# Kernel tuning notes

Measured on AMD Instinct MI355X. Metric: run time of the kernel, lower is better.

Reference implementation:

```python
import jax, jax.numpy as jnp
import numpy as np

N, LH, PL = 512, 20, 10          # agents, history len, prediction len
H, E, NH, FF = 128, 64, 10, 2048  # rnn hidden, embedding, heads, ffn dim
D = H + 2                         # transformer d_model = 130
DH = D // NH                      # head dim = 13
DT = 0.1
NLAYERS = 3


def setup_inputs() -> dict:
    key = jax.random.key(0)
    ks = list(jax.random.split(key, 40))
    def rn(shape, s=0.02):
        return jax.random.normal(ks.pop(), shape, jnp.float32) * s
    Tracks = jax.random.normal(ks.pop(), (N, LH, 5), jnp.float32)
    Tracks = Tracks.at[:, :, 0].set(1.0)  # nonzero ids: all agents active every frame
    return dict(
        Tracks=Tracks,
        W_emb=rn((E, 4)), b_emb=jnp.zeros((E,), jnp.float32),
        W_ih=rn((4 * H, E)), W_hh=rn((4 * H, H)),
        b_ih=jnp.zeros((4 * H,), jnp.float32), b_hh=jnp.zeros((4 * H,), jnp.float32),
        enc_qkv_w=rn((NLAYERS, 3 * D, D)), enc_qkv_b=jnp.zeros((NLAYERS, 3 * D), jnp.float32),
        enc_out_w=rn((NLAYERS, D, D)), enc_out_b=jnp.zeros((NLAYERS, D), jnp.float32),
        enc_ff1_w=rn((NLAYERS, FF, D)), enc_ff1_b=jnp.zeros((NLAYERS, FF), jnp.float32),
        enc_ff2_w=rn((NLAYERS, D, FF)), enc_ff2_b=jnp.zeros((NLAYERS, D), jnp.float32),
        enc_ln1_s=jnp.ones((NLAYERS, D), jnp.float32), enc_ln1_b=jnp.zeros((NLAYERS, D), jnp.float32),
        enc_ln2_s=jnp.ones((NLAYERS, D), jnp.float32), enc_ln2_b=jnp.zeros((NLAYERS, D), jnp.float32),
        W_sp=rn((H, D)), b_sp=jnp.zeros((H,), jnp.float32),
        W_p1=rn((H, H)), b_p1=jnp.zeros((H,), jnp.float32),
        W_p2=rn((H, H)), b_p2=jnp.zeros((H,), jnp.float32),
        W_pl=rn((2, H)), b_pl=jnp.zeros((2,), jnp.float32),
    )


def _ln(x, s, b):
    m = jnp.mean(x, -1, keepdims=True)
    v = jnp.mean((x - m) ** 2, -1, keepdims=True)
    return (x - m) / jnp.sqrt(v + 1e-5) * s + b


def _mha(x, qkv_w, qkv_b, ow, ob):
    # x: [N, D] unbatched sequence of N agent tokens (torch unbatched semantics)
    qkv = x @ qkv_w.T + qkv_b
    q, k, v = jnp.split(qkv, 3, -1)
    def heads(t):
        return t.reshape(-1, NH, DH).transpose(1, 0, 2)  # [NH, N, DH]
    q, k, v = heads(q), heads(k), heads(v)
    scores = jnp.einsum('hnd,hmd->hnm', q, k) / jnp.sqrt(jnp.float32(DH))
    att = jax.nn.softmax(scores, -1)
    o = jnp.einsum('hnm,hmd->hnd', att, v).transpose(1, 0, 2).reshape(-1, D)
    return o @ ow.T + ob


def _forward(Tracks, W_emb, b_emb, W_ih, W_hh, b_ih, b_hh,
             enc_qkv_w, enc_qkv_b, enc_out_w, enc_out_b,
             enc_ff1_w, enc_ff1_b, enc_ff2_w, enc_ff2_b,
             enc_ln1_s, enc_ln1_b, enc_ln2_s, enc_ln2_b,
             W_sp, b_sp, W_p1, b_p1, W_p2, b_p2, W_pl, b_pl):
    def emb(x):
        return x @ W_emb.T + b_emb

    def lstm(x, h, c):  # torch LSTMCell, gate order i,f,g,o
        g = x @ W_ih.T + b_ih + h @ W_hh.T + b_hh
        i, f, gg, o = jnp.split(g, 4, -1)
        c2 = jax.nn.sigmoid(f) * c + jax.nn.sigmoid(i) * jnp.tanh(gg)
        return jax.nn.sigmoid(o) * jnp.tanh(c2), c2

    def sp(h, pos):  # sp_model: 3-layer post-norm transformer encoder + linear
        x = jnp.concatenate([h, pos], 1)  # [N, D]
        for j in range(NLAYERS):
            a = _mha(x, enc_qkv_w[j], enc_qkv_b[j], enc_out_w[j], enc_out_b[j])
            x = _ln(x + a, enc_ln1_s[j], enc_ln1_b[j])
            f = jax.nn.relu(x @ enc_ff1_w[j].T + enc_ff1_b[j]) @ enc_ff2_w[j].T + enc_ff2_b[j]
            x = _ln(x + f, enc_ln2_s[j], enc_ln2_b[j])
        return x @ W_sp.T + b_sp

    def rm_sp(inp, Sh, c):
        h2, c2 = lstm(emb(inp), Sh, c)
        return sp(h2, inp[:, :2]), c2

    n = Tracks.shape[0]
    inp0 = Tracks[:, 0, 1:]
    z = jnp.zeros((n, H), Tracks.dtype)
    h, c = lstm(emb(inp0), z, z)  # step-0 init (original processes step 0 twice)
    Sh = sp(h, inp0[:, :2])

    def step(carry, inp):
        Sh, c = carry
        Sh, c = rm_sp(inp, Sh, c)
        return (Sh, c), None

    (Sh, c), _ = jax.lax.scan(step, (Sh, c), jnp.moveaxis(Tracks[:, :, 1:], 1, 0))

    def pstep(carry, _):
        Sh, c, cf = carry
        x = jax.nn.relu(Sh @ W_p1.T + b_p1) + Sh
        x = jax.nn.relu(x @ W_p2.T + b_p2) + x
        a = x @ W_pl.T + b_pl                       # acceleration [N,2]
        v = a * DT + cf[:, 2:]                      # velocity update first (in-place order)
        pnew = a * (DT * DT / 2) + v * DT + cf[:, :2]
        out = jnp.concatenate([pnew, v], 1)
        Sh, c = rm_sp(out, Sh, c)
        return (Sh, c, out), out

    _, pre = jax.lax.scan(pstep, (Sh, c, Tracks[:, -1, 1:]), None, length=PL)
    return jnp.moveaxis(pre, 0, 1)  # [N, pre_len, 4]


def reference(Tracks, W_emb, b_emb, W_ih, W_hh, b_ih, b_hh,
              enc_qkv_w, enc_qkv_b, enc_out_w, enc_out_b,
              enc_ff1_w, enc_ff1_b, enc_ff2_w, enc_ff2_b,
              enc_ln1_s, enc_ln1_b, enc_ln2_s, enc_ln2_b,
              W_sp, b_sp, W_p1, b_p1, W_p2, b_p2, W_pl, b_pl):
    return _forward(Tracks, W_emb, b_emb, W_ih, W_hh, b_ih, b_hh,
                    enc_qkv_w, enc_qkv_b, enc_out_w, enc_out_b,
                    enc_ff1_w, enc_ff1_b, enc_ff2_w, enc_ff2_b,
                    enc_ln1_s, enc_ln1_b, enc_ln2_s, enc_ln2_b,
                    W_sp, b_sp, W_p1, b_p1, W_p2, b_p2, W_pl, b_pl)
```

## Files before the change

### kernel.cpp

```cpp
#include <hip/hip_runtime.h>


#define Nn 512
#define Dd 130
#define DP 132
#define Hh 128
#define Ee 64
#define FFf 2048
#define KG 192
#define TS 68

typedef float v4 __attribute__((ext_vector_type(4)));
typedef float v2 __attribute__((ext_vector_type(2)));

struct Args {
  const float *Tracks, *W_emb, *b_emb, *W_ih, *W_hh, *b_ih, *b_hh;
  const float *qkv_w, *qkv_b, *out_w, *out_b, *ff1_w, *ff1_b, *ff2_w, *ff2_b;
  const float *ln1_s, *ln1_b, *ln2_s, *ln2_b;
  const float *W_sp, *b_sp, *W_p1, *b_p1, *W_p2, *b_p2, *W_pl, *b_pl;
  float *X, *T, *Q, *Kb, *V, *O, *Sh, *C, *X1, *X2, *Y, *PART, *outp;
};

__device__ __forceinline__ float sigm(float x){ return 1.f/(1.f+__expf(-x)); }

#define LN_REDUCE(SCR) \
  { int row_=tid>>3, l8=tid&7; float s1=0.f, s2=0.f; \
    for (int k=0;k<17;k++){ int c=l8+8*k; if(c<Dd){ float v=(SCR)[row_*132+c]; s1+=v; s2+=v*v; } } \
    red1[row_*9+l8]=s1; red2_[row_*9+l8]=s2; } \
  __syncthreads(); \
  if (tid<64){ float s1=0.f,s2=0.f; \
    for (int k=0;k<8;k++){ s1+=red1[tid*9+k]; s2+=red2_[tid*9+k]; } \
    float m=s1/130.f; mu[tid]=m; inv[tid]=rsqrtf(s2/130.f-m*m+1e-5f); } \
  __syncthreads();

#define GEMM64(KK) \
  float acc[2][4] = {}; \
  { const float* xp = xs + 2*ig; \
    const float* wp = ws + 4*cg; \
    _Pragma("unroll 4") \
    for (int j=0;j<(KK);j++){ \
      v2 xv = *(const v2*)(xp + j*TS); \
      v4 wv = *(const v4*)(wp + j*TS); \
      _Pragma("unroll") \
      for (int aa=0;aa<2;aa++) \
        _Pragma("unroll") \
        for (int bb=0;bb<4;bb++) acc[aa][bb] += xv[aa]*wv[bb]; \
    } }

__global__ __launch_bounds__(512) void k_proj(Args a){
  int rg = blockIdx.x & 7, cs = blockIdx.x >> 3;
  int r0 = rg*64, c0 = cs*64;
  __shared__ alignas(16) float xs[Dd*TS];
  __shared__ alignas(16) float ws[Dd*TS];
  __shared__ float row[64*132];
  __shared__ float red1[64*9], red2_[64*9], mu[64], inv[64];
  int tid = threadIdx.x, cg = tid & 15, ig = tid >> 4;
  const float* f2b = a.ff2_b + 2*Dd;
  const float* lns = a.ln2_s + 2*Dd;
  const float* lnb = a.ln2_b + 2*Dd;
  for (int idx=tid; idx<64*Dd; idx+=512){ int c=idx/Dd, j=idx-c*Dd; ws[j*TS+c] = a.W_sp[(c0+c)*Dd+j]; }
  for (int idx=tid; idx<64*Dd; idx+=512){ int i=idx/Dd, j=idx-i*Dd;
    float sum = a.X[(r0+i)*DP+j] + f2b[j];
    for (int ksl=0;ksl<16;ksl++) sum += a.PART[(ksl*Nn + r0+i)*DP + j];
    row[i*132+j] = sum; }
  __syncthreads();
  LN_REDUCE(row)
  for (int idx=tid; idx<64*Dd; idx+=512){ int i=idx/Dd, j=idx-i*Dd;
    xs[j*TS+i] = (row[i*132+j]-mu[i])*inv[i]*lns[j] + lnb[j]; }
  __syncthreads();
  GEMM64(Dd)
  #pragma unroll
  for (int aa=0;aa<2;aa++){
    int r = r0 + 2*ig + aa, c = c0 + 4*cg;
    v4 o;
    #pragma unroll
    for (int bb=0;bb<4;bb++) o[bb] = acc[aa][bb] + a.b_sp[c+bb];
    *(v4*)&a.Sh[r*Hh+c] = o;
  }
}

__global__ __launch_bounds__(512) void k_tail(Args a, int p){
  int r0 = blockIdx.x*64;
  __shared__ alignas(16) float xs[Dd*TS];
  __shared__ alignas(16) float ws[Dd*TS];
  __shared__ float A[64*132];
  __shared__ float B[64*132];
  __shared__ float red1[64*9], red2_[64*9], mu[64], inv[64];
  __shared__ float pr[32*17];
  int tid = threadIdx.x, cg = tid & 15, ig = tid >> 4;
  const float* f2b = a.ff2_b + 2*Dd;
  const float* lns = a.ln2_s + 2*Dd;
  const float* lnb = a.ln2_b + 2*Dd;
  for (int idx=tid; idx<64*Dd; idx+=512){ int i=idx/Dd, j=idx-i*Dd;
    float sum = a.X[(r0+i)*DP+j] + f2b[j];
    for (int ksl=0;ksl<16;ksl++) sum += a.PART[(ksl*Nn + r0+i)*DP + j];
    A[i*132+j] = sum; }
  __syncthreads();
  LN_REDUCE(A)
  for (int idx=tid; idx<64*Dd; idx+=512){ int i=idx/Dd, j=idx-i*Dd;
    xs[j*TS+i] = (A[i*132+j]-mu[i])*inv[i]*lns[j] + lnb[j]; }
  __syncthreads();
  for (int cc=0; cc<2; cc++){
    for (int idx=tid; idx<64*Dd; idx+=512){ int c=idx/Dd, j=idx-c*Dd;
      ws[j*TS+c] = a.W_sp[(cc*64+c)*Dd+j]; }
    __syncthreads();
    GEMM64(Dd)
    __syncthreads();
    #pragma unroll
    for (int aa=0;aa<2;aa++){
      int rl = 2*ig + aa, c = cc*64 + 4*cg;
      v4 o;
      #pragma unroll
      for (int bb=0;bb<4;bb++) o[bb] = acc[aa][bb] + a.b_sp[c+bb];
      *(v4*)&A[rl*132+c] = o;
      *(v4*)&a.Sh[(r0+rl)*Hh+c] = o;
    }
    __syncthreads();
  }
  for (int m=0;m<2;m++){
    const float* W  = m ? a.W_p2 : a.W_p1;
    const float* bi = m ? a.b_p2 : a.b_p1;
    float* src = m ? B : A;
    float* dst = m ? A : B;
    for (int idx=tid; idx<64*Hh; idx+=512){ int i=idx>>7, j=idx&127; xs[j*TS+i]=src[i*132+j]; }
    __syncthreads();
    for (int cc=0; cc<2; cc++){
      for (int idx=tid; idx<64*Hh; idx+=512){ int c=idx>>7, j=idx&127;
        ws[j*TS+c] = W[(cc*64+c)*Hh+j]; }
      __syncthreads();
      GEMM64(Hh)
      __syncthreads();
      #pragma unroll
      for (int aa=0;aa<2;aa++){
        int rl = 2*ig + aa, c = cc*64 + 4*cg;
        #pragma unroll
        for (int bb=0;bb<4;bb++)
          dst[rl*132+c+bb] = fmaxf(acc[aa][bb]+bi[c+bb],0.f) + src[rl*132+c+bb];
      }
      __syncthreads();
    }
    __syncthreads();
  }
  for (int sub=0; sub<4; sub++){
    int o2 = tid & 31, kq = tid >> 5;
    int ii2 = o2>>1, jj = o2&1;
    int rl = sub*16 + ii2;
    float s = 0.f;
    for (int v=kq*8; v<kq*8+8; v++) s += A[rl*132+v]*a.W_pl[jj*Hh+v];
    pr[o2*17+kq] = s;
    __syncthreads();
    if (tid < 32){
      int oo=tid, i2=oo>>1, j=oo&1, rr=r0+sub*16+i2;
      float av = a.b_pl[j];
      for (int k=0;k<16;k++) av += pr[oo*17+k];
      float cf0, cf2;
      if (p==0){ cf0 = a.Tracks[(rr*20+19)*5+1+j]; cf2 = a.Tracks[(rr*20+19)*5+3+j]; }
      else     { cf0 = a.outp[rr*40+(p-1)*4+j];    cf2 = a.outp[rr*40+(p-1)*4+2+j]; }
      float vv = av*0.1f + cf2;
      float pn = av*0.005f + vv*0.1f + cf0;
      a.outp[rr*40+p*4+j]   = pn;
      a.outp[rr*40+p*4+2+j] = vv;
    }
    __syncthreads();
  }
}

__global__ __launch_bounds__(512) void k_gates(Args a, int xin_mode, int tstep, int p, int sh_zero){
  int rg = blockIdx.x & 7, us = blockIdx.x >> 3;
  int r0 = rg*64, u0 = us*16;
  __shared__ alignas(16) float xs[KG*TS];
  __shared__ alignas(16) float ws[KG*TS];
  __shared__ float xin[64*4];
  int tid = threadIdx.x, cg = tid & 15, ig = tid >> 4;
  for (int idx=tid; idx<64*4; idx+=512){ int i=idx>>2, j=idx&3; int r=r0+i;
    xin[i*4+j] = (xin_mode==0) ? a.Tracks[(r*20+tstep)*5+1+j] : a.outp[r*40+p*4+j]; }
  for (int idx=tid; idx<64*Hh; idx+=512){ int i=idx>>7, v=idx&127;
    xs[(Ee+v)*TS+i] = sh_zero ? 0.f : a.Sh[(r0+i)*Hh+v]; }
  for (int idx=tid; idx<64*KG; idx+=512){ int row=idx/KG, j=idx-row*KG;
    int u=row>>2, g=row&3; int wrow = g*Hh + u0 + u;
    ws[j*TS+row] = (j<Ee) ? a.W_ih[wrow*Ee+j] : a.W_hh[wrow*Hh+(j-Ee)]; }
  __syncthreads();
  for (int idx=tid; idx<64*Ee; idx+=512){ int e=idx>>6, i=idx&63;
    float s = a.b_emb[e];
    #pragma unroll
    for (int j=0;j<4;j++) s += xin[i*4+j]*a.W_emb[e*4+j];
    xs[e*TS+i] = s; }
  __syncthreads();
  GEMM64(KG)
  int u = u0 + cg;
  #pragma unroll
  for (int rr=0;rr<2;rr++){
    int r = r0 + 2*ig + rr;
    float gi = acc[rr][0] + a.b_ih[u]      + a.b_hh[u];
    float gf = acc[rr][1] + a.b_ih[Hh+u]   + a.b_hh[Hh+u];
    float gg = acc[rr][2] + a.b_ih[2*Hh+u] + a.b_hh[2*Hh+u];
    float go = acc[rr][3] + a.b_ih[3*Hh+u] + a.b_hh[3*Hh+u];
    float cp = sh_zero ? 0.f : a.C[r*Hh+u];
    float c2 = sigm(gf)*cp + sigm(gi)*tanhf(gg);
    a.C[r*Hh+u] = c2;
    a.X[r*DP+u] = sigm(go)*tanhf(c2);
  }
  if (us==0 && tid<128){ int i=tid>>1, jj=tid&1;
    a.X[(r0+i)*DP + Hh + jj] = xin[i*4+jj]; }
}

__global__ __launch_bounds__(512) void k_qkv(Args a, int layer){
  int rg = blockIdx.x & 7, cs = blockIdx.x >> 3;
  int r0 = rg*64, c0 = cs*64;
  __shared__ alignas(16) float xs[Dd*TS];
  __shared__ alignas(16) float ws[Dd*TS];
  const float* qw = a.qkv_w + layer*390*Dd;
  const float* qb = a.qkv_b + layer*390;
  int tid = threadIdx.x, cg = tid & 15, ig = tid >> 4;
  for (int idx=tid; idx<64*Dd; idx+=512){ int i=idx/Dd, j=idx-i*Dd; xs[j*TS+i] = a.X[(r0+i)*DP+j]; }
  for (int idx=tid; idx<64*Dd; idx+=512){ int c=idx/Dd, j=idx-c*Dd; int gc=c0+c;
    ws[j*TS+c] = (gc<390) ? qw[gc*Dd+j] : 0.f; }
  __syncthreads();
  GEMM64(Dd)
  #pragma unroll
  for (int aa=0;aa<2;aa++){
    int r = r0 + 2*ig + aa;
    #pragma unroll
    for (int bb=0;bb<4;bb++){
      int c = c0 + 4*cg + bb;
      if (c < 390){
        float v = acc[aa][bb] + qb[c];
        if (c < Dd)        a.Q [r*DP + c]        = v;
        else if (c < 2*Dd) a.Kb[r*DP + (c-Dd)]   = v;
        else               a.V [r*DP + (c-2*Dd)] = v;
      }
    }
  }
}

__global__ __launch_bounds__(256) void k_attn(Args a){
  int rg = blockIdx.x & 31, head = blockIdx.x >> 5;
  int r0 = rg*16, hc = head*13;
  __shared__ alignas(16) float Ks[512*14];
  __shared__ alignas(16) float Vs[512*14];
  __shared__ float red[16*17];
  __shared__ float rowm[16], rowsi[16];
  __shared__ float red2[256*13];
  int tid = threadIdx.x;
  const float scale = rsqrtf(13.f);
  for (int idx=tid; idx<512*13; idx+=256){ int m=idx/13, d=idx-13*m; Ks[m*14+d]=a.Kb[m*DP+hc+d]; }
  for (int idx=tid; idx<512*13; idx+=256){ int m=idx/13, d=idx-13*m; Vs[m*14+d]=a.V[m*DP+hc+d]; }
  __syncthreads();
  int ii = tid>>4, mg = tid&15;
  float q[13];
  #pragma unroll
  for (int d=0;d<13;d++) q[d]=a.Q[(r0+ii)*DP+hc+d]*scale;
  float p[32];
  #pragma unroll
  for (int k=0;k<32;k++){ int m=mg+16*k;
    float s=0.f;
    #pragma unroll
    for (int d=0;d<13;d++) s += q[d]*Ks[m*14+d];
    p[k]=s; }
  { float mx=-1e30f;
    #pragma unroll
    for (int k=0;k<32;k++) mx=fmaxf(mx,p[k]);
    red[ii*17+mg]=mx; }
  __syncthreads();
  if (tid<16){ float mx=-1e30f; for(int k=0;k<16;k++) mx=fmaxf(mx,red[tid*17+k]); rowm[tid]=mx; }
  __syncthreads();
  { float mx=rowm[ii]; float s=0.f;
    #pragma unroll
    for (int k=0;k<32;k++){ float e=__expf(p[k]-mx); p[k]=e; s+=e; }
    red[ii*17+mg]=s; }
  __syncthreads();
  if (tid<16){ float s=0.f; for(int k=0;k<16;k++) s+=red[tid*17+k]; rowsi[tid]=1.f/s; }
  float po[13];
  #pragma unroll
  for (int d=0;d<13;d++) po[d]=0.f;
  #pragma unroll
  for (int k=0;k<32;k++){ int m=mg+16*k;
    float pv = p[k];
    #pragma unroll
    for (int d=0;d<13;d++) po[d] += pv*Vs[m*14+d];
  }
  #pragma unroll
  for (int d=0;d<13;d++) red2[tid*13+d]=po[d];
  __syncthreads();
  if (tid<208){ int i2=tid/13, d=tid-13*i2;
    float acc=0.f;
    for (int l=0;l<16;l++) acc += red2[(i2*16+l)*13+d];
    a.O[(r0+i2)*DP+hc+d]=acc*rowsi[i2]; }
}

__global__ __launch_bounds__(512) void k_oproj(Args a, int layer){
  int rg = blockIdx.x & 7, cs = blockIdx.x >> 3;
  int r0 = rg*64, c0 = cs*64;
  __shared__ alignas(16) float xs[Dd*TS];
  __shared__ alignas(16) float ws[Dd*TS];
  const float* ow = a.out_w + layer*Dd*Dd;
  const float* ob = a.out_b + layer*Dd;
  int tid = threadIdx.x, cg = tid & 15, ig = tid >> 4;
  for (int idx=tid; idx<64*Dd; idx+=512){ int i=idx/Dd, j=idx-i*Dd; xs[j*TS+i]=a.O[(r0+i)*DP+j]; }
  for (int idx=tid; idx<64*Dd; idx+=512){ int c=idx/Dd, j=idx-c*Dd; int gc=c0+c;
    ws[j*TS+c] = (gc<Dd) ? ow[gc*Dd+j] : 0.f; }
  __syncthreads();
  GEMM64(Dd)
  #pragma unroll
  for (int aa=0;aa<2;aa++){
    int r = r0 + 2*ig + aa;
    #pragma unroll
    for (int bb=0;bb<4;bb++){
      int c = c0 + 4*cg + bb;
      if (c < Dd) a.T[r*DP+c] = acc[aa][bb] + ob[c] + a.X[r*DP+c];
    }
  }
}

__global__ __launch_bounds__(256) void k_ln(Args a, const float* s, const float* b, int layer){
  int r0 = blockIdx.x*8;
  __shared__ float row[8*132];
  __shared__ float red1[8*33], red2[8*33];
  __shared__ float mu[8], inv[8];
  int tid = threadIdx.x, i = tid>>5, l = tid&31;
  const float* f2b = a.ff2_b + layer*Dd;
  for (int idx=tid; idx<8*Dd; idx+=256){ int ii=idx/Dd, c=idx-ii*Dd;
    float sum = a.X[(r0+ii)*DP+c] + f2b[c];
    for (int ksl=0;ksl<16;ksl++) sum += a.PART[(ksl*Nn + r0+ii)*DP + c];
    row[ii*132+c]=sum; }
  __syncthreads();
  { float s1=0.f, s2=0.f;
    for (int k=0;k<5;k++){ int c=l+32*k; if(c<Dd){ float v=row[i*132+c]; s1+=v; s2+=v*v; } }
    red1[i*33+l]=s1; red2[i*33+l]=s2; }
  __syncthreads();
  if (tid<8){ float s1=0.f,s2=0.f; for(int k=0;k<32;k++){ s1+=red1[tid*33+k]; s2+=red2[tid*33+k]; }
    float m=s1/130.f; mu[tid]=m; inv[tid]=rsqrtf(s2/130.f - m*m + 1e-5f); }
  __syncthreads();
  for (int idx=tid; idx<8*Dd; idx+=256){ int ii=idx/Dd, c=idx-ii*Dd;
    a.X[(r0+ii)*DP+c] = (row[ii*132+c]-mu[ii])*inv[ii]*s[c] + b[c]; }
}

__global__ __launch_bounds__(512) void k_ff1(Args a, int layer){
  int rg = blockIdx.x & 7, cs = blockIdx.x >> 3;
  int r0 = rg*64, c0 = cs*64;
  __shared__ alignas(16) float xs[Dd*TS];
  __shared__ alignas(16) float ws[Dd*TS];
  __shared__ float red1[64*9], red2_[64*9], mu[64], inv[64];
  const float* w1 = a.ff1_w + layer*FFf*Dd;
  const float* b1 = a.ff1_b + layer*FFf;
  const float* lns = a.ln1_s + layer*Dd;
  const float* lnb = a.ln1_b + layer*Dd;
  int tid = threadIdx.x, cg = tid & 15, ig = tid >> 4;
  for (int idx=tid; idx<64*Dd; idx+=512){ int c=idx/Dd, j=idx-c*Dd; ws[j*TS+c]=w1[(c0+c)*Dd+j]; }
  { int row_=tid>>3, l8=tid&7; float s1=0.f, s2=0.f;
    const float* tr = a.T + (r0+row_)*DP;
    for (int k=0;k<17;k++){ int c=l8+8*k; if(c<Dd){ float v=tr[c]; s1+=v; s2+=v*v; } }
    red1[row_*9+l8]=s1; red2_[row_*9+l8]=s2; }
  __syncthreads();
  if (tid<64){ float s1=0.f,s2=0.f;
    for (int k=0;k<8;k++){ s1+=red1[tid*9+k]; s2+=red2_[tid*9+k]; }
    float m=s1/130.f; mu[tid]=m; inv[tid]=rsqrtf(s2/130.f-m*m+1e-5f); }
  __syncthreads();
  for (int idx=tid; idx<64*Dd; idx+=512){ int i=idx/Dd, j=idx-i*Dd;
    float v = (a.T[(r0+i)*DP+j]-mu[i])*inv[i]*lns[j] + lnb[j];
    xs[j*TS+i] = v;
    if (cs==0) a.X[(r0+i)*DP+j] = v; }
  __syncthreads();
  GEMM64(Dd)
  #pragma unroll
  for (int aa=0;aa<2;aa++){
    int r = r0 + 2*ig + aa, c = c0 + 4*cg;
    v4 o;
    #pragma unroll
    for (int bb=0;bb<4;bb++) o[bb] = fmaxf(acc[aa][bb]+b1[c+bb],0.f);
    *(v4*)&a.Y[r*FFf+c] = o;
  }
}

__global__ __launch_bounds__(512) void k_ff2(Args a, int layer){
  int b = blockIdx.x;
  int rg = b & 7; int t = b >> 3; int ks = t/3; int cs = t - ks*3;
  int r0 = rg*64, c0 = cs*64, k0 = ks*128;
  __shared__ alignas(16) float xs[128*TS];
  __shared__ alignas(16) float ws[128*TS];
  const float* w2 = a.ff2_w + layer*Dd*FFf;
  int tid = threadIdx.x, cg = tid & 15, ig = tid >> 4;
  for (int idx=tid; idx<64*128; idx+=512){ int i=idx>>7, j=idx&127; xs[j*TS+i]=a.Y[(r0+i)*FFf+k0+j]; }
  for (int idx=tid; idx<64*128; idx+=512){ int c=idx>>7, j=idx&127; int gc=c0+c;
    ws[j*TS+c] = (gc<Dd) ? w2[gc*FFf+k0+j] : 0.f; }
  __syncthreads();
  GEMM64(128)
  #pragma unroll
  for (int aa=0;aa<2;aa++){
    int r = r0 + 2*ig + aa;
    #pragma unroll
    for (int bb=0;bb<4;bb++){
      int c = c0 + 4*cg + bb;
      if (c < Dd) a.PART[(ks*Nn + r)*DP + c] = acc[aa][bb];
    }
  }
}

extern "C" void kernel_launch(void* const* d_in, const int* in_sizes, int n_in,
                              void* d_out, int out_size, void* d_ws, size_t ws_size,
                              hipStream_t stream) {
  (void)in_sizes; (void)n_in; (void)out_size; (void)ws_size;
  Args A;
  const float* const* in = (const float* const*)d_in;
  A.Tracks=in[0]; A.W_emb=in[1]; A.b_emb=in[2]; A.W_ih=in[3]; A.W_hh=in[4]; A.b_ih=in[5]; A.b_hh=in[6];
  A.qkv_w=in[7]; A.qkv_b=in[8]; A.out_w=in[9]; A.out_b=in[10];
  A.ff1_w=in[11]; A.ff1_b=in[12]; A.ff2_w=in[13]; A.ff2_b=in[14];
  A.ln1_s=in[15]; A.ln1_b=in[16]; A.ln2_s=in[17]; A.ln2_b=in[18];
  A.W_sp=in[19]; A.b_sp=in[20]; A.W_p1=in[21]; A.b_p1=in[22]; A.W_p2=in[23]; A.b_p2=in[24];
  A.W_pl=in[25]; A.b_pl=in[26];
  float* ws = (float*)d_ws;
  A.X   = ws;
  A.T   = ws + 67584;
  A.Q   = ws + 135168;
  A.Kb  = ws + 202752;
  A.V   = ws + 270336;
  A.O   = ws + 337920;
  A.Sh  = ws + 405504;
  A.C   = ws + 471040;
  A.X1  = ws + 536576;
  A.X2  = ws + 602112;
  A.Y   = ws + 667648;
  A.PART= ws + 1716224;
  A.outp = (float*)d_out;

  dim3 B5(512), B2(256);
  auto enc = [&](){
    for (int l=0;l<3;l++){
      k_qkv  <<<dim3(56),  B5, 0, stream>>>(A, l);
      k_attn <<<dim3(320), B2, 0, stream>>>(A);
      k_oproj<<<dim3(24),  B5, 0, stream>>>(A, l);
      k_ff1  <<<dim3(256), B5, 0, stream>>>(A, l);
      k_ff2  <<<dim3(384), B5, 0, stream>>>(A, l);
      if (l < 2)
        k_ln <<<dim3(64),  B2, 0, stream>>>(A, A.ln2_s+l*Dd, A.ln2_b+l*Dd, l);
    }
  };

  k_gates<<<dim3(64), B5, 0, stream>>>(A, 0, 0, 0, 1);
  enc();
  for (int t=0;t<20;t++){
    k_proj <<<dim3(16), B5, 0, stream>>>(A);
    k_gates<<<dim3(64), B5, 0, stream>>>(A, 0, t, 0, 0);
    enc();
  }
  for (int p=0;p<10;p++){
    k_tail<<<dim3(8), B5, 0, stream>>>(A, p);
    if (p < 9){
      k_gates<<<dim3(64), B5, 0, stream>>>(A, 1, 0, p, 0);
      enc();
    }
  }
}
```

Before: 8.922 ms.

## Split prediction tail into parallel kernels and widen attention blocks

The single 8-block k_tail kernel, which ran LN, the spatial projection, two residual MLPs and the output head serially, is replaced by separate launches: k_proj (16 blocks), two k_mlp launches (16 blocks each) and k_pout (64 blocks). This spreads the tail work over more CUs at the cost of extra launches and global round trips. Attention now runs 512 threads per block, each thread handling 16 keys instead of 32, and reuses the K/V shared memory for the partial-sum buffer. The aim is more parallelism per block and lower shared-memory footprint.

```diff
diff --git a/kernel.cpp b/kernel.cpp
--- a/kernel.cpp
+++ b/kernel.cpp
@@ -79,89 +79,48 @@
   }
 }
 
-__global__ __launch_bounds__(512) void k_tail(Args a, int p){
-  int r0 = blockIdx.x*64;
-  __shared__ alignas(16) float xs[Dd*TS];
-  __shared__ alignas(16) float ws[Dd*TS];
-  __shared__ float A[64*132];
-  __shared__ float B[64*132];
-  __shared__ float red1[64*9], red2_[64*9], mu[64], inv[64];
-  __shared__ float pr[32*17];
-  int tid = threadIdx.x, cg = tid & 15, ig = tid >> 4;
-  const float* f2b = a.ff2_b + 2*Dd;
-  const float* lns = a.ln2_s + 2*Dd;
-  const float* lnb = a.ln2_b + 2*Dd;
-  for (int idx=tid; idx<64*Dd; idx+=512){ int i=idx/Dd, j=idx-i*Dd;
-    float sum = a.X[(r0+i)*DP+j] + f2b[j];
-    for (int ksl=0;ksl<16;ksl++) sum += a.PART[(ksl*Nn + r0+i)*DP + j];
-    A[i*132+j] = sum; }
-  __syncthreads();
-  LN_REDUCE(A)
-  for (int idx=tid; idx<64*Dd; idx+=512){ int i=idx/Dd, j=idx-i*Dd;
-    xs[j*TS+i] = (A[i*132+j]-mu[i])*inv[i]*lns[j] + lnb[j]; }
-  __syncthreads();
-  for (int cc=0; cc<2; cc++){
-    for (int idx=tid; idx<64*Dd; idx+=512){ int c=idx/Dd, j=idx-c*Dd;
-      ws[j*TS+c] = a.W_sp[(cc*64+c)*Dd+j]; }
-    __syncthreads();
-    GEMM64(Dd)
-    __syncthreads();
-    #pragma unroll
-    for (int aa=0;aa<2;aa++){
-      int rl = 2*ig + aa, c = cc*64 + 4*cg;
-      v4 o;
-      #pragma unroll
-      for (int bb=0;bb<4;bb++) o[bb] = acc[aa][bb] + a.b_sp[c+bb];
-      *(v4*)&A[rl*132+c] = o;
-      *(v4*)&a.Sh[(r0+rl)*Hh+c] = o;
-    }
-    __syncthreads();
-  }
-  for (int m=0;m<2;m++){
-    const float* W  = m ? a.W_p2 : a.W_p1;
-    const float* bi = m ? a.b_p2 : a.b_p1;
-    float* src = m ? B : A;
-    float* dst = m ? A : B;
-    for (int idx=tid; idx<64*Hh; idx+=512){ int i=idx>>7, j=idx&127; xs[j*TS+i]=src[i*132+j]; }
-    __syncthreads();
-    for (int cc=0; cc<2; cc++){
-      for (int idx=tid; idx<64*Hh; idx+=512){ int c=idx>>7, j=idx&127;
-        ws[j*TS+c] = W[(cc*64+c)*Hh+j]; }
-      __syncthreads();
-      GEMM64(Hh)
-      __syncthreads();
-      #pragma unroll
-      for (int aa=0;aa<2;aa++){
-        int rl = 2*ig + aa, c = cc*64 + 4*cg;
-        #pragma unroll
-        for (int bb=0;bb<4;bb++)
-          dst[rl*132+c+bb] = fmaxf(acc[aa][bb]+bi[c+bb],0.f) + src[rl*132+c+bb];
-      }
-      __syncthreads();
-    }
-    __syncthreads();
-  }
-  for (int sub=0; sub<4; sub++){
-    int o2 = tid & 31, kq = tid >> 5;
-    int ii2 = o2>>1, jj = o2&1;
-    int rl = sub*16 + ii2;
-    float s = 0.f;
-    for (int v=kq*8; v<kq*8+8; v++) s += A[rl*132+v]*a.W_pl[jj*Hh+v];
-    pr[o2*17+kq] = s;
-    __syncthreads();
-    if (tid < 32){
-      int oo=tid, i2=oo>>1, j=oo&1, rr=r0+sub*16+i2;
-      float av = a.b_pl[j];
-      for (int k=0;k<16;k++) av += pr[oo*17+k];
-      float cf0, cf2;
-      if (p==0){ cf0 = a.Tracks[(rr*20+19)*5+1+j]; cf2 = a.Tracks[(rr*20+19)*5+3+j]; }
-      else     { cf0 = a.outp[rr*40+(p-1)*4+j];    cf2 = a.outp[rr*40+(p-1)*4+2+j]; }
-      float vv = av*0.1f + cf2;
-      float pn = av*0.005f + vv*0.1f + cf0;
-      a.outp[rr*40+p*4+j]   = pn;
-      a.outp[rr*40+p*4+2+j] = vv;
-    }
-    __syncthreads();
+__global__ __launch_bounds__(512) void k_mlp(Args a, const float* inp, const float* W, const float* b, float* outp){
+  int rg = blockIdx.x & 7, cs = blockIdx.x >> 3;
+  int r0 = rg*64, c0 = cs*64;
+  __shared__ alignas(16) float xs[Hh*TS];
+  __shared__ alignas(16) float ws[Hh*TS];
+  int tid = threadIdx.x, cg = tid & 15, ig = tid >> 4;
+  for (int idx=tid; idx<64*Hh; idx+=512){ int i=idx>>7, j=idx&127; xs[j*TS+i] = inp[(r0+i)*Hh+j]; }
+  for (int idx=tid; idx<64*Hh; idx+=512){ int c=idx>>7, j=idx&127; ws[j*TS+c] = W[(c0+c)*Hh+j]; }
+  __syncthreads();
+  GEMM64(Hh)
+  #pragma unroll
+  for (int aa=0;aa<2;aa++){
+    int r = r0 + 2*ig + aa, c = c0 + 4*cg;
+    v4 ri = *(const v4*)&inp[r*Hh+c];
+    v4 o;
+    #pragma unroll
+    for (int bb=0;bb<4;bb++) o[bb] = fmaxf(acc[aa][bb]+b[c+bb],0.f) + ri[bb];
+    *(v4*)&outp[r*Hh+c] = o;
+  }
+}
+
+__global__ __launch_bounds__(256) void k_pout(Args a, int p){
+  int r0 = blockIdx.x*8;
+  __shared__ float red[16*17];
+  int tid = threadIdx.x;
+  int o = tid & 15, kq = tid >> 4;
+  int ii = o>>1, jj = o&1, r = r0+ii;
+  float s = 0.f;
+  for (int v=kq*8; v<kq*8+8; v++) s += a.X2[r*Hh+v]*a.W_pl[jj*Hh+v];
+  red[o*17+kq] = s;
+  __syncthreads();
+  if (tid < 16){
+    int oo=tid, i2=oo>>1, j=oo&1, rr=r0+i2;
+    float av = a.b_pl[j];
+    for (int k=0;k<16;k++) av += red[oo*17+k];
+    float cf0, cf2;
+    if (p==0){ cf0 = a.Tracks[(rr*20+19)*5+1+j]; cf2 = a.Tracks[(rr*20+19)*5+3+j]; }
+    else     { cf0 = a.outp[rr*40+(p-1)*4+j];    cf2 = a.outp[rr*40+(p-1)*4+2+j]; }
+    float vv = av*0.1f + cf2;
+    float pn = av*0.005f + vv*0.1f + cf0;
+    a.outp[rr*40+p*4+j]   = pn;
+    a.outp[rr*40+p*4+2+j] = vv;
   }
 }
 
@@ -233,58 +192,61 @@
   }
 }
 
-__global__ __launch_bounds__(256) void k_attn(Args a){
+__global__ __launch_bounds__(512) void k_attn(Args a){
   int rg = blockIdx.x & 31, head = blockIdx.x >> 5;
   int r0 = rg*16, hc = head*13;
-  __shared__ alignas(16) float Ks[512*14];
-  __shared__ alignas(16) float Vs[512*14];
-  __shared__ float red[16*17];
-  __shared__ float rowm[16], rowsi[16];
-  __shared__ float red2[256*13];
+  __shared__ alignas(16) float smem[7168 + 7168 + 528 + 32];
+  float* Ks   = smem;
+  float* Vs   = smem + 7168;
+  float* red  = smem + 14336;
+  float* rowm = smem + 14864;
+  float* rowsi= smem + 14880;
+  float* red2 = smem;
   int tid = threadIdx.x;
   const float scale = rsqrtf(13.f);
-  for (int idx=tid; idx<512*13; idx+=256){ int m=idx/13, d=idx-13*m; Ks[m*14+d]=a.Kb[m*DP+hc+d]; }
-  for (int idx=tid; idx<512*13; idx+=256){ int m=idx/13, d=idx-13*m; Vs[m*14+d]=a.V[m*DP+hc+d]; }
-  __syncthreads();
-  int ii = tid>>4, mg = tid&15;
+  for (int idx=tid; idx<512*13; idx+=512){ int m=idx/13, d=idx-13*m; Ks[m*14+d]=a.Kb[m*DP+hc+d]; }
+  for (int idx=tid; idx<512*13; idx+=512){ int m=idx/13, d=idx-13*m; Vs[m*14+d]=a.V[m*DP+hc+d]; }
+  __syncthreads();
+  int ii = tid>>5, mg = tid&31;
   float q[13];
   #pragma unroll
   for (int d=0;d<13;d++) q[d]=a.Q[(r0+ii)*DP+hc+d]*scale;
-  float p[32];
-  #pragma unroll
-  for (int k=0;k<32;k++){ int m=mg+16*k;
+  float p[16];
+  #pragma unroll
+  for (int k=0;k<16;k++){ int m=mg+32*k;
     float s=0.f;
     #pragma unroll
     for (int d=0;d<13;d++) s += q[d]*Ks[m*14+d];
     p[k]=s; }
   { float mx=-1e30f;
     #pragma unroll
-    for (int k=0;k<32;k++) mx=fmaxf(mx,p[k]);
-    red[ii*17+mg]=mx; }
-  __syncthreads();
-  if (tid<16){ float mx=-1e30f; for(int k=0;k<16;k++) mx=fmaxf(mx,red[tid*17+k]); rowm[tid]=mx; }
+    for (int k=0;k<16;k++) mx=fmaxf(mx,p[k]);
+    red[ii*33+mg]=mx; }
+  __syncthreads();
+  if (tid<16){ float mx=-1e30f; for(int k=0;k<32;k++) mx=fmaxf(mx,red[tid*33+k]); rowm[tid]=mx; }
   __syncthreads();
   { float mx=rowm[ii]; float s=0.f;
     #pragma unroll
-    for (int k=0;k<32;k++){ float e=__expf(p[k]-mx); p[k]=e; s+=e; }
-    red[ii*17+mg]=s; }
-  __syncthreads();
-  if (tid<16){ float s=0.f; for(int k=0;k<16;k++) s+=red[tid*17+k]; rowsi[tid]=1.f/s; }
+    for (int k=0;k<16;k++){ float e=__expf(p[k]-mx); p[k]=e; s+=e; }
+    red[ii*33+mg]=s; }
+  __syncthreads();
+  if (tid<16){ float s=0.f; for(int k=0;k<32;k++) s+=red[tid*33+k]; rowsi[tid]=1.f/s; }
   float po[13];
   #pragma unroll
   for (int d=0;d<13;d++) po[d]=0.f;
   #pragma unroll
-  for (int k=0;k<32;k++){ int m=mg+16*k;
+  for (int k=0;k<16;k++){ int m=mg+32*k;
     float pv = p[k];
     #pragma unroll
     for (int d=0;d<13;d++) po[d] += pv*Vs[m*14+d];
   }
+  __syncthreads();
   #pragma unroll
   for (int d=0;d<13;d++) red2[tid*13+d]=po[d];
   __syncthreads();
   if (tid<208){ int i2=tid/13, d=tid-13*i2;
     float acc=0.f;
-    for (int l=0;l<16;l++) acc += red2[(i2*16+l)*13+d];
+    for (int l=0;l<32;l++) acc += red2[(i2*32+l)*13+d];
     a.O[(r0+i2)*DP+hc+d]=acc*rowsi[i2]; }
 }
 
@@ -427,7 +389,7 @@
   auto enc = [&](){
     for (int l=0;l<3;l++){
       k_qkv  <<<dim3(56),  B5, 0, stream>>>(A, l);
-      k_attn <<<dim3(320), B2, 0, stream>>>(A);
+      k_attn <<<dim3(320), B5, 0, stream>>>(A);
       k_oproj<<<dim3(24),  B5, 0, stream>>>(A, l);
       k_ff1  <<<dim3(256), B5, 0, stream>>>(A, l);
       k_ff2  <<<dim3(384), B5, 0, stream>>>(A, l);
@@ -444,7 +406,10 @@
     enc();
   }
   for (int p=0;p<10;p++){
-    k_tail<<<dim3(8), B5, 0, stream>>>(A, p);
+    k_proj<<<dim3(16), B5, 0, stream>>>(A);
+    k_mlp <<<dim3(16), B5, 0, stream>>>(A, A.Sh, A.W_p1, A.b_p1, A.X1);
+    k_mlp <<<dim3(16), B5, 0, stream>>>(A, A.X1, A.W_p2, A.b_p2, A.X2);
+    k_pout<<<dim3(64), B2, 0, stream>>>(A, p);
     if (p < 9){
       k_gates<<<dim3(64), B5, 0, stream>>>(A, 1, 0, p, 0);
       enc();
```

Result: slower. 9.405 ms (+5.4%).
